# Optimization experiments

Measured on AMD Instinct MI355X. Metric: run time of the kernel, lower is better.

The kernel has to match this reference:

```python
import jax, jax.numpy as jnp
import numpy as np

IN_F = 4096
OUT_F = 4096
THRESH = 0.1

def setup_inputs() -> dict:
    key = jax.random.key(0)
    kx, kw = jax.random.split(key)
    x = jax.random.normal(kx, (4, 2048, IN_F), dtype=jnp.float32)
    weight = jax.random.normal(kw, (OUT_F, IN_F), dtype=jnp.float32) * 0.5
    bias = jnp.zeros((OUT_F,), dtype=jnp.float32)
    return {"x": x, "weight": weight, "bias": bias}

def reference(x, weight, bias):
    # ternary quantization: sign(w) where |w| > 0.1, else 0
    q = jnp.sign(weight) * (jnp.abs(weight) > THRESH).astype(weight.dtype)
    # straight-through estimator: forward uses q, gradient flows to weight
    w_ste = weight + jax.lax.stop_gradient(q - weight)
    # F.linear: x @ w_ste.T + bias
    return jnp.einsum('bsi,oi->bso', x, w_ste) + bias
```

## Files before the change

### kernel.cpp

```cpp
#include <hip/hip_runtime.h>
#include <cstdint>
#include <cstddef>

#define MDIM 8192
#define NDIM 4096
#define KDIM 4096
#define TERN_THRESH 0.1f

typedef unsigned short u16;
typedef __bf16 bf16x8 __attribute__((ext_vector_type(8)));
typedef float f32x4 __attribute__((ext_vector_type(4)));
typedef u16 u16x4 __attribute__((ext_vector_type(4)));
typedef u16 u16x8 __attribute__((ext_vector_type(8)));


__device__ __forceinline__ u16 f2bf(float f) {
  unsigned u = __float_as_uint(f);
  u += 0x7FFFu + ((u >> 16) & 1u);
  return (u16)(u >> 16);
}

__device__ __forceinline__ u16 tern_bf16(float w) {
  return w > TERN_THRESH ? (u16)0x3F80u : (w < -TERN_THRESH ? (u16)0xBF80u : (u16)0u);
}

__device__ __forceinline__ void load_lds16(const u16* g, u16* s) {
  __builtin_amdgcn_global_load_lds(
      (__attribute__((address_space(1))) void*)(void*)(g),
      (__attribute__((address_space(3))) void*)(void*)(s),
      16, 0, 0);
}


#define XBLOCKS ((MDIM * (size_t)KDIM) / (8 * 256))
#define WBLOCKS ((NDIM * (size_t)KDIM) / (8 * 256))

__global__ __launch_bounds__(256) void cvt_kernel(const float* __restrict__ x,
                                                  u16* __restrict__ xb,
                                                  const float* __restrict__ w,
                                                  u16* __restrict__ qb) {
  size_t b = blockIdx.x;
  if (b < XBLOCKS) {
    size_t i0 = b * 512 + threadIdx.x;
    size_t i1 = i0 + 256;
    const f32x4* x4 = (const f32x4*)x;
    f32x4 a = __builtin_nontemporal_load(&x4[i0]);
    f32x4 c = __builtin_nontemporal_load(&x4[i1]);
    u16x4 oa, oc;
    oa[0] = f2bf(a[0]); oa[1] = f2bf(a[1]); oa[2] = f2bf(a[2]); oa[3] = f2bf(a[3]);
    oc[0] = f2bf(c[0]); oc[1] = f2bf(c[1]); oc[2] = f2bf(c[2]); oc[3] = f2bf(c[3]);
    ((u16x4*)xb)[i0] = oa;
    ((u16x4*)xb)[i1] = oc;
  } else {
    size_t i0 = (b - XBLOCKS) * 512 + threadIdx.x;
    size_t i1 = i0 + 256;
    const f32x4* w4 = (const f32x4*)w;
    f32x4 a = __builtin_nontemporal_load(&w4[i0]);
    f32x4 c = __builtin_nontemporal_load(&w4[i1]);
    u16x4 oa, oc;
    oa[0] = tern_bf16(a[0]); oa[1] = tern_bf16(a[1]); oa[2] = tern_bf16(a[2]); oa[3] = tern_bf16(a[3]);
    oc[0] = tern_bf16(c[0]); oc[1] = tern_bf16(c[1]); oc[2] = tern_bf16(c[2]); oc[3] = tern_bf16(c[3]);
    ((u16x4*)qb)[i0] = oa;
    ((u16x4*)qb)[i1] = oc;
  }
}


#define NTILE (KDIM / 32)

#define BARRIER() __builtin_amdgcn_s_barrier()
#define FENCE()   asm volatile("" ::: "memory")
#define VMCNT4()  asm volatile("s_waitcnt vmcnt(4)" ::: "memory")

#define MFMA16(AF, BF, I0)                                                   \
  do {                                                                       \
    _Pragma("unroll") for (int _i = 0; _i < 4; ++_i) {                       \
      _Pragma("unroll") for (int _j = 0; _j < 4; ++_j) {                     \
        acc[(I0) + _i][_j] = __builtin_amdgcn_mfma_f32_16x16x32_bf16(        \
            AF[_i], BF[_j], acc[(I0) + _i][_j], 0, 0, 0);                    \
      }                                                                      \
    }                                                                        \
  } while (0)

__global__ __launch_bounds__(512, 2) void gemm_tern_kernel(
    const u16* __restrict__ Xb,
    const u16* __restrict__ Qb,
    const float* __restrict__ bias,
    float* __restrict__ C) {
  __shared__ __attribute__((aligned(16))) u16 As[4 * 8192];
  __shared__ __attribute__((aligned(16))) u16 Bs[4 * 8192];

  const int tid  = threadIdx.x;
  const int lane = tid & 63;
  const int wv   = tid >> 6;
  const int wm   = wv >> 2;
  const int wn   = wv & 3;
  const int quad = lane >> 4;
  const int l16  = lane & 15;

  const int orig    = blockIdx.y * 16 + blockIdx.x;
  const int wg      = (orig & 7) * 64 + (orig >> 3);
  const int rowBase = (wg >> 4) * 256;
  const int colBase = (wg & 15) * 256;

  const u16* gA[2];
  const u16* gB[2];
  int sOff[2];
#pragma unroll
  for (int j = 0; j < 2; ++j) {
    int c  = j * 512 + tid;
    int r  = c >> 2;
    int qg = (c & 3) ^ ((r >> 1) & 3);
    gA[j]   = Xb + (size_t)(rowBase + r) * KDIM + qg * 8;
    gB[j]   = Qb + (size_t)(colBase + r) * KDIM + qg * 8;
    sOff[j] = c * 8;
  }

#define STAGE_A(s, kt)                                              \
  do {                                                              \
    load_lds16(gA[0] + (kt), (u16*)As + (s) * 8192 + sOff[0]);      \
    load_lds16(gA[1] + (kt), (u16*)As + (s) * 8192 + sOff[1]);      \
  } while (0)
#define STAGE_B(s, kt)                                              \
  do {                                                              \
    load_lds16(gB[0] + (kt), (u16*)Bs + (s) * 8192 + sOff[0]);      \
    load_lds16(gB[1] + (kt), (u16*)Bs + (s) * 8192 + sOff[1]);      \
  } while (0)

  int ac[8], bc[4];
#pragma unroll
  for (int i = 0; i < 8; ++i) {
    int r = wm * 128 + i * 16 + l16;
    ac[i] = (r * 4 + (quad ^ ((r >> 1) & 3))) * 8;
  }
#pragma unroll
  for (int j = 0; j < 4; ++j) {
    int r = wn * 64 + j * 16 + l16;
    bc[j] = (r * 4 + (quad ^ ((r >> 1) & 3))) * 8;
  }

#define RD_A(d, i, s) d = *(const bf16x8*)((const u16*)As + (s) * 8192 + ac[i])
#define RD_B(d, j, s) d = *(const bf16x8*)((const u16*)Bs + (s) * 8192 + bc[j])

  f32x4 acc[8][4] = {};
  bf16x8 a0[4], b0[4], a1[4], b1[4], ab[4];

  STAGE_A(0, 0);  STAGE_B(0, 0);
  STAGE_A(1, 32); STAGE_B(1, 32);
  STAGE_A(2, 64); STAGE_B(2, 64);
  VMCNT4();
  FENCE(); BARRIER(); FENCE();
  RD_A(a0[0], 0, 0); RD_A(a0[1], 1, 0); RD_A(a0[2], 2, 0); RD_A(a0[3], 3, 0);
  RD_B(b0[0], 0, 0); RD_B(b0[1], 1, 0); RD_B(b0[2], 2, 0); RD_B(b0[3], 3, 0);

#define TILE(S, AC, BC, AN, BN, PRE)                                       \
  do {                                                                     \
    const int kt = (t + 3 < NTILE) ? (t + 3) * 32 : 0;                     \
    RD_A(ab[0], 4, S); RD_A(ab[1], 5, S);                                  \
    RD_A(ab[2], 6, S); RD_A(ab[3], 7, S);                                  \
    STAGE_A(((S) + 3) & 3, kt);                                            \
    __builtin_amdgcn_s_setprio(1);                                         \
    MFMA16(AC, BC, 0);                                                     \
    __builtin_amdgcn_s_setprio(0);                                         \
    if (PRE) {                                                             \
      RD_A(AN[0], 0, ((S) + 1) & 3); RD_A(AN[1], 1, ((S) + 1) & 3);        \
      RD_A(AN[2], 2, ((S) + 1) & 3); RD_A(AN[3], 3, ((S) + 1) & 3);        \
      RD_B(BN[0], 0, ((S) + 1) & 3); RD_B(BN[1], 1, ((S) + 1) & 3);        \
      RD_B(BN[2], 2, ((S) + 1) & 3); RD_B(BN[3], 3, ((S) + 1) & 3);        \
    }                                                                      \
    STAGE_B(((S) + 3) & 3, kt);                                            \
    __builtin_amdgcn_s_setprio(1);                                         \
    MFMA16(ab, BC, 4);                                                     \
    __builtin_amdgcn_s_setprio(0);                                         \
    VMCNT4();                                                              \
    FENCE(); BARRIER(); FENCE();                                           \
    ++t;                                                                   \
  } while (0)

  int t = 0;
  for (int it = 0; it < NTILE / 4 - 1; ++it) {
    TILE(0, a0, b0, a1, b1, 1);
    TILE(1, a1, b1, a0, b0, 1);
    TILE(2, a0, b0, a1, b1, 1);
    TILE(3, a1, b1, a0, b0, 1);
  }
  TILE(0, a0, b0, a1, b1, 1);
  TILE(1, a1, b1, a0, b0, 1);
  TILE(2, a0, b0, a1, b1, 1);
  TILE(3, a1, b1, a0, b0, 0);

  float bv[4];
#pragma unroll
  for (int j = 0; j < 4; ++j) bv[j] = bias[colBase + wn * 64 + j * 16 + l16];

#pragma unroll
  for (int i = 0; i < 8; ++i) {
#pragma unroll
    for (int r = 0; r < 4; ++r) {
      int grow = rowBase + wm * 128 + i * 16 + quad * 4 + r;
      float* crow = C + (size_t)grow * NDIM + colBase + wn * 64 + l16;
#pragma unroll
      for (int j = 0; j < 4; ++j) {
        crow[j * 16] = acc[i][j][r] + bv[j];
      }
    }
  }
}


extern "C" void kernel_launch(void* const* d_in, const int* in_sizes, int n_in,
                              void* d_out, int out_size, void* d_ws, size_t ws_size,
                              hipStream_t stream) {
  const float* x    = (const float*)d_in[0];
  const float* w    = (const float*)d_in[1];
  const float* bias = (const float*)d_in[2];
  float* out = (float*)d_out;

  u16* xb = (u16*)d_ws;
  u16* qb = xb + (size_t)MDIM * KDIM;

  cvt_kernel<<<(unsigned)(XBLOCKS + WBLOCKS), 256, 0, stream>>>(x, xb, w, qb);

  dim3 grid(NDIM / 256, MDIM / 256);
  gemm_tern_kernel<<<grid, 512, 0, stream>>>(xb, qb, bias, out);
}
```

Baseline: 460.9 us.

## Load ternary weight fragments directly from global into registers, bypassing LDS

Removes the LDS staging buffer for the B (ternary weight) operand. Each wave now loads its B fragments straight from global memory into registers one tile ahead, and the vmcnt waits are adjusted to match the new count of outstanding loads. This halves LDS usage and drops the LDS writes and reads for B. In exchange it adds redundant global/L2 traffic, since waves sharing a column slice each fetch the same B data, and it risks exposed global latency because B is prefetched only one tile ahead. The conversion kernel also switches from nontemporal loads to plain loads.

Result: slower. 652.8 us (+41.6%).

```diff
diff --git a/kernel.cpp b/kernel.cpp
--- a/kernel.cpp
+++ b/kernel.cpp
@@ -44,8 +44,8 @@
     size_t i0 = b * 512 + threadIdx.x;
     size_t i1 = i0 + 256;
     const f32x4* x4 = (const f32x4*)x;
-    f32x4 a = __builtin_nontemporal_load(&x4[i0]);
-    f32x4 c = __builtin_nontemporal_load(&x4[i1]);
+    f32x4 a = x4[i0];
+    f32x4 c = x4[i1];
     u16x4 oa, oc;
     oa[0] = f2bf(a[0]); oa[1] = f2bf(a[1]); oa[2] = f2bf(a[2]); oa[3] = f2bf(a[3]);
     oc[0] = f2bf(c[0]); oc[1] = f2bf(c[1]); oc[2] = f2bf(c[2]); oc[3] = f2bf(c[3]);
@@ -55,8 +55,8 @@
     size_t i0 = (b - XBLOCKS) * 512 + threadIdx.x;
     size_t i1 = i0 + 256;
     const f32x4* w4 = (const f32x4*)w;
-    f32x4 a = __builtin_nontemporal_load(&w4[i0]);
-    f32x4 c = __builtin_nontemporal_load(&w4[i1]);
+    f32x4 a = w4[i0];
+    f32x4 c = w4[i1];
     u16x4 oa, oc;
     oa[0] = tern_bf16(a[0]); oa[1] = tern_bf16(a[1]); oa[2] = tern_bf16(a[2]); oa[3] = tern_bf16(a[3]);
     oc[0] = tern_bf16(c[0]); oc[1] = tern_bf16(c[1]); oc[2] = tern_bf16(c[2]); oc[3] = tern_bf16(c[3]);
@@ -70,7 +70,8 @@
 
 #define BARRIER() __builtin_amdgcn_s_barrier()
 #define FENCE()   asm volatile("" ::: "memory")
-#define VMCNT4()  asm volatile("s_waitcnt vmcnt(4)" ::: "memory")
+#define VMCNT6()  asm volatile("s_waitcnt vmcnt(6)" ::: "memory")
+#define VMCNT8()  asm volatile("s_waitcnt vmcnt(8)" ::: "memory")
 
 #define MFMA16(AF, BF, I0)                                                   \
   do {                                                                       \
@@ -88,7 +89,6 @@
     const float* __restrict__ bias,
     float* __restrict__ C) {
   __shared__ __attribute__((aligned(16))) u16 As[4 * 8192];
-  __shared__ __attribute__((aligned(16))) u16 Bs[4 * 8192];
 
   const int tid  = threadIdx.x;
   const int lane = tid & 63;
@@ -104,7 +104,6 @@
   const int colBase = (wg & 15) * 256;
 
   const u16* gA[2];
-  const u16* gB[2];
   int sOff[2];
 #pragma unroll
   for (int j = 0; j < 2; ++j) {
@@ -112,7 +111,6 @@
     int r  = c >> 2;
     int qg = (c & 3) ^ ((r >> 1) & 3);
     gA[j]   = Xb + (size_t)(rowBase + r) * KDIM + qg * 8;
-    gB[j]   = Qb + (size_t)(colBase + r) * KDIM + qg * 8;
     sOff[j] = c * 8;
   }
 
@@ -121,58 +119,62 @@
     load_lds16(gA[0] + (kt), (u16*)As + (s) * 8192 + sOff[0]);      \
     load_lds16(gA[1] + (kt), (u16*)As + (s) * 8192 + sOff[1]);      \
   } while (0)
-#define STAGE_B(s, kt)                                              \
+
+  const u16* gB[4];
+#pragma unroll
+  for (int j = 0; j < 4; ++j) {
+    gB[j] = Qb + (size_t)(colBase + wn * 64 + j * 16 + l16) * KDIM + quad * 8;
+  }
+
+#define LOAD_B(BN, kt)                                              \
   do {                                                              \
-    load_lds16(gB[0] + (kt), (u16*)Bs + (s) * 8192 + sOff[0]);      \
-    load_lds16(gB[1] + (kt), (u16*)Bs + (s) * 8192 + sOff[1]);      \
-  } while (0)
-
-  int ac[8], bc[4];
+    BN[0] = *(const bf16x8*)(gB[0] + (kt));                         \
+    BN[1] = *(const bf16x8*)(gB[1] + (kt));                         \
+    BN[2] = *(const bf16x8*)(gB[2] + (kt));                         \
+    BN[3] = *(const bf16x8*)(gB[3] + (kt));                         \
+  } while (0)
+
+  int ac[8];
 #pragma unroll
   for (int i = 0; i < 8; ++i) {
     int r = wm * 128 + i * 16 + l16;
     ac[i] = (r * 4 + (quad ^ ((r >> 1) & 3))) * 8;
   }
-#pragma unroll
-  for (int j = 0; j < 4; ++j) {
-    int r = wn * 64 + j * 16 + l16;
-    bc[j] = (r * 4 + (quad ^ ((r >> 1) & 3))) * 8;
-  }
 
 #define RD_A(d, i, s) d = *(const bf16x8*)((const u16*)As + (s) * 8192 + ac[i])
-#define RD_B(d, j, s) d = *(const bf16x8*)((const u16*)Bs + (s) * 8192 + bc[j])
 
   f32x4 acc[8][4] = {};
-  bf16x8 a0[4], b0[4], a1[4], b1[4], ab[4];
-
-  STAGE_A(0, 0);  STAGE_B(0, 0);
-  STAGE_A(1, 32); STAGE_B(1, 32);
-  STAGE_A(2, 64); STAGE_B(2, 64);
-  VMCNT4();
+  bf16x8 a0[4], a1[4], ab[4], b0[4], b1[4];
+
+  STAGE_A(0, 0);
+  STAGE_A(1, 32);
+  STAGE_A(2, 64);
+  FENCE();
+  LOAD_B(b0, 0);
+  VMCNT8();
   FENCE(); BARRIER(); FENCE();
   RD_A(a0[0], 0, 0); RD_A(a0[1], 1, 0); RD_A(a0[2], 2, 0); RD_A(a0[3], 3, 0);
-  RD_B(b0[0], 0, 0); RD_B(b0[1], 1, 0); RD_B(b0[2], 2, 0); RD_B(b0[3], 3, 0);
 
 #define TILE(S, AC, BC, AN, BN, PRE)                                       \
   do {                                                                     \
-    const int kt = (t + 3 < NTILE) ? (t + 3) * 32 : 0;                     \
+    const int kt  = (t + 3 < NTILE) ? (t + 3) * 32 : 0;                    \
+    const int kbn = (t + 1 < NTILE) ? (t + 1) * 32 : 0;                    \
+    STAGE_A(((S) + 3) & 3, kt);                                            \
+    FENCE();                                                               \
+    LOAD_B(BN, kbn);                                                       \
     RD_A(ab[0], 4, S); RD_A(ab[1], 5, S);                                  \
     RD_A(ab[2], 6, S); RD_A(ab[3], 7, S);                                  \
-    STAGE_A(((S) + 3) & 3, kt);                                            \
     __builtin_amdgcn_s_setprio(1);                                         \
     MFMA16(AC, BC, 0);                                                     \
     __builtin_amdgcn_s_setprio(0);                                         \
     if (PRE) {                                                             \
       RD_A(AN[0], 0, ((S) + 1) & 3); RD_A(AN[1], 1, ((S) + 1) & 3);        \
       RD_A(AN[2], 2, ((S) + 1) & 3); RD_A(AN[3], 3, ((S) + 1) & 3);        \
-      RD_B(BN[0], 0, ((S) + 1) & 3); RD_B(BN[1], 1, ((S) + 1) & 3);        \
-      RD_B(BN[2], 2, ((S) + 1) & 3); RD_B(BN[3], 3, ((S) + 1) & 3);        \
     }                                                                      \
-    STAGE_B(((S) + 3) & 3, kt);                                            \
     __builtin_amdgcn_s_setprio(1);                                         \
     MFMA16(ab, BC, 4);                                                     \
     __builtin_amdgcn_s_setprio(0);                                         \
-    VMCNT4();                                                              \
+    VMCNT6();                                                              \
     FENCE(); BARRIER(); FENCE();                                           \
     ++t;                                                                   \
   } while (0)
```
